# Performance work log

Measured on AMD Instinct MI355X. Metric: run time of the kernel, lower is better.

Reference implementation:

```python
import jax, jax.numpy as jnp
import numpy as np

B, C, H = 16, 512, 8
T_PI, T_P = 2048, 512  # mel frames, text tokens


def setup_inputs() -> dict:
    key = jax.random.key(0)
    ks = jax.random.split(key, 8)
    pi = jax.random.uniform(ks[0], (B, T_PI), dtype=jnp.float32) * T_P  # mel positions in text coords
    p = jax.random.uniform(ks[1], (B, T_P), dtype=jnp.float32) * T_P   # text positions
    x_h = jax.random.normal(ks[2], (B, C, T_P), dtype=jnp.float32)
    text_mask = jnp.ones((B, T_P), dtype=bool)
    sigma = jnp.ones((H,), dtype=jnp.float32) * 0.1
    w_hidden = jax.random.normal(ks[3], (2 * C, C), dtype=jnp.float32) / np.sqrt(C)
    b_hidden = jnp.zeros((2 * C,), dtype=jnp.float32)
    w_out = jax.random.normal(ks[4], (C, 2 * C), dtype=jnp.float32) / np.sqrt(2 * C)
    b_out = jnp.zeros((C,), dtype=jnp.float32)
    return {"pi": pi, "p": p, "x_h": x_h, "text_mask": text_mask,
            "sigma": sigma, "w_hidden": w_hidden, "b_hidden": b_hidden,
            "w_out": w_out, "b_out": b_out}


def reference(pi, p, x_h, text_mask, sigma, w_hidden, b_hidden, w_out, b_out):
    # Gaussian position-distance energies: (B, T_pi, T_p)
    energies = -(pi[:, :, None] - p[:, None, :]) ** 2
    real_sigma = jnp.clip(sigma, 1e-6, 3.0)  # (H,)
    # scale per head -> (B, H, T_pi, T_p)
    energies = energies[:, None, :, :] * real_sigma[None, :, None, None]
    energies = jnp.where(text_mask[:, None, None, :], energies, -jnp.inf)
    attns = jax.nn.softmax(energies, axis=-1)  # (B, H, T_pi, T_p)

    # 1x1 conv C -> 2C: h (B, 2C, T_p)
    h = jnp.einsum('oc,bct->bot', w_hidden, x_h) + b_hidden[None, :, None]
    Bh, twoC, Tp = h.shape
    nH = real_sigma.shape[0]
    d = twoC // nH
    h = h.reshape(Bh, nH, d, Tp).transpose(0, 1, 3, 2)  # (B, H, T_p, d)

    out = jnp.einsum('bhqt,bhtd->bhqd', attns, h)        # (B, H, T_pi, d)
    out = out.transpose(0, 1, 3, 2).reshape(Bh, twoC, -1)  # (B, 2C, T_pi)
    out = jnp.einsum('oc,bct->bot', w_out, out) + b_out[None, :, None]  # (B, C, T_pi)
    return (out, attns, real_sigma)
```

## Files before the change

kernel.cpp:

```cpp
#include <hip/hip_runtime.h>
#include <stdint.h>


typedef float  f32x4  __attribute__((ext_vector_type(4)));
typedef short  bf16x8 __attribute__((ext_vector_type(8)));

namespace {
constexpr int Bn = 16, Cc = 512, Hh = 8, TQ = 2048, TP = 512, Dd = 128, C2 = 1024;
constexpr size_t ATT_OFF = (size_t)Bn * Cc * TQ;
constexpr size_t SIG_OFF = ATT_OFF + (size_t)Bn * Hh * TQ * TP;
constexpr size_t XT_ELEMS  = (size_t)Bn * TP * Cc;
constexpr size_t WHB_ELEMS = (size_t)C2 * Cc;
constexpr size_t WOB_ELEMS = (size_t)Cc * C2;
constexpr size_t HWS_ELEMS = (size_t)Bn * Hh * Dd * TP;
constexpr size_t YWS_ELEMS = (size_t)Bn * TQ * C2;
}

__device__ inline ushort f2bf(float f) {
    uint32_t u = __float_as_uint(f);
    u += 0x7FFFu + ((u >> 16) & 1u);
    return (ushort)(u >> 16);
}

__device__ inline void gload16(const ushort* g, ushort* l) {
    __builtin_amdgcn_global_load_lds(
        (const __attribute__((address_space(1))) uint32_t*)g,
        (__attribute__((address_space(3))) uint32_t*)l, 16, 0, 0);
}

__global__ __launch_bounds__(256) void k_prep(
    const float* __restrict__ wh, const float* __restrict__ wo,
    const float* __restrict__ sg,
    ushort* __restrict__ whb, ushort* __restrict__ wob, float* __restrict__ sigo)
{
    int i = blockIdx.x * 256 + threadIdx.x;
    float4 a = *reinterpret_cast<const float4*>(&wh[(size_t)i * 4]);
    float4 b = *reinterpret_cast<const float4*>(&wo[(size_t)i * 4]);
    ushort4 ua, ub;
    ua.x = f2bf(a.x); ua.y = f2bf(a.y); ua.z = f2bf(a.z); ua.w = f2bf(a.w);
    ub.x = f2bf(b.x); ub.y = f2bf(b.y); ub.z = f2bf(b.z); ub.w = f2bf(b.w);
    *reinterpret_cast<ushort4*>(&whb[(size_t)i * 4]) = ua;
    *reinterpret_cast<ushort4*>(&wob[(size_t)i * 4]) = ub;
    if (i < Hh) sigo[i] = fminf(fmaxf(sg[i], 1e-6f), 3.0f);
}

__global__ __launch_bounds__(256) void k_xt(
    const float* __restrict__ x, ushort* __restrict__ xT)
{
    __shared__ float tile[64 * 67];
    int bid = blockIdx.x;
    int tt = bid & 7, cb = (bid >> 3) & 7, b = bid >> 6;
    int c0 = cb * 64, t0 = tt * 64;
    int tid = threadIdx.x;
    #pragma unroll
    for (int it = 0; it < 4; ++it) {
        int idx = it * 256 + tid;
        int rc = idx >> 4, tc = (idx & 15) * 4;
        float4 v = *reinterpret_cast<const float4*>(
            &x[((size_t)b * Cc + c0 + rc) * TP + t0 + tc]);
        tile[rc * 67 + tc + 0] = v.x; tile[rc * 67 + tc + 1] = v.y;
        tile[rc * 67 + tc + 2] = v.z; tile[rc * 67 + tc + 3] = v.w;
    }
    __syncthreads();
    #pragma unroll
    for (int it = 0; it < 4; ++it) {
        int idx = it * 256 + tid;
        int rt = idx >> 4, cc = (idx & 15) * 4;
        ushort4 o;
        o.x = f2bf(tile[(cc + 0) * 67 + rt]);
        o.y = f2bf(tile[(cc + 1) * 67 + rt]);
        o.z = f2bf(tile[(cc + 2) * 67 + rt]);
        o.w = f2bf(tile[(cc + 3) * 67 + rt]);
        *reinterpret_cast<ushort4*>(&xT[((size_t)b * TP + t0 + rt) * Cc + c0 + cc]) = o;
    }
}


__device__ __forceinline__ void hidden_role(
    int hid, ushort* pool, int tid,
    const ushort* xT, const ushort* whb, const float* bias, ushort* hws)
{
    int l = tid & 63, w = tid >> 6;
    int ot = hid & 15, tt = (hid >> 4) & 7, b = hid >> 7;
    int o0 = ot * 64, t0 = tt * 64;
    ushort* As = pool;
    ushort* Bs = pool + 4096;
    float* bias_s = reinterpret_cast<float*>(pool + 8192);
    if (tid < 64) bias_s[tid] = bias[o0 + tid];

    int wn = w * 16;
    int r = l & 15, g = l >> 4;
    f32x4 acc[4];
    #pragma unroll
    for (int m = 0; m < 4; ++m) acc[m] = (f32x4){0.f, 0.f, 0.f, 0.f};

    const ushort* ag = xT + ((size_t)b * TP + t0) * Cc;
    const ushort* bg = whb + (size_t)o0 * Cc;

    for (int k0 = 0; k0 < Cc; k0 += 64) {
        __syncthreads();
        #pragma unroll
        for (int it = 0; it < 2; ++it) {
            int idx = it * 256 + tid;
            int row = idx >> 3, ch = idx & 7;
            int dst = row * 64 + ((ch ^ (row & 7)) * 8);
            *reinterpret_cast<bf16x8*>(&As[dst]) =
                *reinterpret_cast<const bf16x8*>(&ag[(size_t)row * Cc + k0 + ch * 8]);
            *reinterpret_cast<bf16x8*>(&Bs[dst]) =
                *reinterpret_cast<const bf16x8*>(&bg[(size_t)row * Cc + k0 + ch * 8]);
        }
        __syncthreads();
        #pragma unroll
        for (int s = 0; s < 2; ++s) {
            int brow = wn + r;
            bf16x8 bv = *reinterpret_cast<const bf16x8*>(
                &Bs[brow * 64 + (((s * 4 + g) ^ (brow & 7)) * 8)]);
            #pragma unroll
            for (int m = 0; m < 4; ++m) {
                int row = m * 16 + r;
                bf16x8 av = *reinterpret_cast<const bf16x8*>(
                    &As[row * 64 + (((s * 4 + g) ^ (row & 7)) * 8)]);
                acc[m] = __builtin_amdgcn_mfma_f32_16x16x32_bf16(av, bv, acc[m], 0, 0, 0);
            }
        }
    }
    int og = o0 + wn + r;
    int hh = og >> 7, d = og & 127;
    float bi = bias_s[wn + r];
    #pragma unroll
    for (int m = 0; m < 4; ++m) {
        int t = t0 + m * 16 + g * 4;
        ushort4 v;
        v.x = f2bf(acc[m][0] + bi); v.y = f2bf(acc[m][1] + bi);
        v.z = f2bf(acc[m][2] + bi); v.w = f2bf(acc[m][3] + bi);
        *reinterpret_cast<ushort4*>(&hws[(((size_t)b * Hh + hh) * Dd + d) * TP + t]) = v;
    }
}

__device__ __forceinline__ void attw_role(
    int sub, int bbase, ushort* pool, int tid,
    const float* pi, const float* p, const float* sgm,
    float* attns, float2* nrm)
{
    float* p_s   = reinterpret_cast<float*>(pool);
    float* pim_s = reinterpret_cast<float*>(pool) + 512;
    int l = tid & 63, w = tid >> 6;
    int qt = sub & 31, hh = (sub >> 5) & 7, b = bbase + (sub >> 8);
    int q0 = qt * 64;
    float sig = fminf(fmaxf(sgm[hh], 1e-6f), 3.0f), nsig = -sig;

    for (int i = tid; i < TP; i += 256) p_s[i] = p[(size_t)b * TP + i];
    if (tid < 64) pim_s[tid] = pi[(size_t)b * TQ + q0 + tid];
    __syncthreads();

    float* abase = attns + (((size_t)b * Hh + hh) * TQ + q0) * TP;
    float2* nbase = nrm + ((size_t)b * Hh + hh) * TQ + q0;

    for (int rr = 0; rr < 16; ++rr) {
        int qloc = w * 16 + rr;
        float piq = pim_s[qloc];
        float d2[8];
        #pragma unroll
        for (int i = 0; i < 8; ++i) { float df = piq - p_s[l + 64 * i]; d2[i] = df * df; }
        float dmin = d2[0];
        #pragma unroll
        for (int i = 1; i < 8; ++i) dmin = fminf(dmin, d2[i]);
        #pragma unroll
        for (int off = 32; off; off >>= 1) dmin = fminf(dmin, __shfl_xor(dmin, off));
        float negm = sig * dmin;
        float vv[8], ssum = 0.f;
        #pragma unroll
        for (int i = 0; i < 8; ++i) { vv[i] = __expf(fmaf(d2[i], nsig, negm)); ssum += vv[i]; }
        #pragma unroll
        for (int off = 32; off; off >>= 1) ssum += __shfl_xor(ssum, off);
        float inv = 1.0f / ssum;
        if (l == 0) nbase[qloc] = make_float2(negm, inv);
        float* aptr = abase + (size_t)qloc * TP + l;
        #pragma unroll
        for (int i = 0; i < 8; ++i)
            __builtin_nontemporal_store(vv[i] * inv, &aptr[64 * i]);
    }
}

__device__ __forceinline__ void pv_role(
    int sub, int bbase, ushort* pool, int tid,
    const float* pi, const float* p, const float* sgm,
    const ushort* hws, const float2* nrm, ushort* y)
{
    float* p_s    = reinterpret_cast<float*>(pool);
    float* pim_s  = reinterpret_cast<float*>(pool + 1024);
    float* negm_s = reinterpret_cast<float*>(pool + 1152);
    float* inv_s  = reinterpret_cast<float*>(pool + 1280);
    ushort* Ht    = pool + 1408;
    ushort* yst_b = pool + 1408;

    int l = tid & 63, w = tid >> 6;
    int qt = sub & 31, hh = (sub >> 5) & 7, b = bbase + (sub >> 8);
    int q0 = qt * 64;
    float sig = fminf(fmaxf(sgm[hh], 1e-6f), 3.0f), nsig = -sig;

    const ushort* hb = hws + (size_t)(b * Hh + hh) * Dd * TP;
    int srow = l >> 3, sch = l & 7;

    for (int i = tid; i < TP; i += 256) p_s[i] = p[(size_t)b * TP + i];
    if (tid < 64) {
        pim_s[tid] = pi[(size_t)b * TQ + q0 + tid];
        float2 nv = nrm[((size_t)b * Hh + hh) * TQ + q0 + tid];
        negm_s[tid] = nv.x; inv_s[tid] = nv.y;
    }
    __syncthreads();

    int r = l & 15, g = l >> 4;
    int qloc = w * 16 + r;
    float piq = pim_s[qloc], negm = negm_s[qloc];
    f32x4 acc[8];
    #pragma unroll
    for (int n = 0; n < 8; ++n) acc[n] = (f32x4){0.f, 0.f, 0.f, 0.f};

    for (int tt = 0; tt < TP; tt += 64) {
        __syncthreads();
        #pragma unroll
        for (int it = 0; it < 4; ++it) {
            int c = w + it * 4;
            int row = c * 8 + srow;
            int chs = sch ^ (row & 7);
            gload16(&hb[(size_t)row * TP + tt + chs * 8], &Ht[c * 512]);
        }
        __syncthreads();
        #pragma unroll
        for (int s = 0; s < 2; ++s) {
            int tb = tt + s * 32 + g * 8;
            float4 pv0 = *reinterpret_cast<const float4*>(&p_s[tb]);
            float4 pv1 = *reinterpret_cast<const float4*>(&p_s[tb + 4]);
            float pvv[8] = {pv0.x, pv0.y, pv0.z, pv0.w, pv1.x, pv1.y, pv1.z, pv1.w};
            bf16x8 af;
            #pragma unroll
            for (int j = 0; j < 8; ++j) {
                float df = piq - pvv[j];
                af[j] = (short)f2bf(__expf(fmaf(df * df, nsig, negm)));
            }
            #pragma unroll
            for (int n = 0; n < 8; ++n) {
                int row = n * 16 + r;
                bf16x8 bv = *reinterpret_cast<const bf16x8*>(
                    &Ht[row * 64 + (((s * 4 + g) ^ (row & 7)) * 8)]);
                acc[n] = __builtin_amdgcn_mfma_f32_16x16x32_bf16(af, bv, acc[n], 0, 0, 0);
            }
        }
    }
    __syncthreads();

    float inv4[4];
    #pragma unroll
    for (int j = 0; j < 4; ++j) inv4[j] = inv_s[w * 16 + g * 4 + j];
    ushort* yst = yst_b + w * (16 * 132);
    #pragma unroll
    for (int n = 0; n < 8; ++n)
        #pragma unroll
        for (int j = 0; j < 4; ++j)
            yst[(g * 4 + j) * 132 + n * 16 + r] = f2bf(acc[n][j] * inv4[j]);
    __syncthreads();
    size_t ybase = (size_t)b * TQ + q0 + w * 16;
    #pragma unroll
    for (int it = 0; it < 4; ++it) {
        int idx = it * 64 + l;
        int qr = idx >> 4, c8 = (idx & 15) * 8;
        *reinterpret_cast<bf16x8*>(&y[(ybase + qr) * C2 + hh * Dd + c8]) =
            *reinterpret_cast<const bf16x8*>(&yst_b[w * (16 * 132) + qr * 132 + c8]);
    }
}

__device__ __forceinline__ void out_role(
    int oid, int bbase, ushort* pool, int tid,
    const ushort* y, const ushort* wob, const float* bout, float* outp)
{
    ushort* As = pool;
    ushort* Bs = pool + 8192;
    float* bo_s = reinterpret_cast<float*>(pool + 16384);

    int no = oid & 3, mq = (oid >> 2) & 15, b = bbase + (oid >> 6);
    int q0 = mq * 128, o0 = no * 128;
    int l = tid & 63, w = tid >> 6;
    int wm = (w >> 1) * 64, wn = (w & 1) * 64;
    int r = l & 15, g = l >> 4;
    if (tid < 128) bo_s[tid] = bout[o0 + tid];

    int srow = (l >> 3);
    int sch  = l & 7;

    f32x4 acc[4][4];
    #pragma unroll
    for (int m = 0; m < 4; ++m)
        #pragma unroll
        for (int n = 0; n < 4; ++n) acc[m][n] = (f32x4){0.f, 0.f, 0.f, 0.f};

    const ushort* agbase = y + ((size_t)b * TQ + q0) * C2;
    const ushort* bgbase = wob + (size_t)o0 * C2;

    for (int k0 = 0; k0 < C2; k0 += 64) {
        __syncthreads();
        #pragma unroll
        for (int it = 0; it < 4; ++it) {
            int c = w + it * 4;
            int row = c * 8 + srow;
            int chs = sch ^ (row & 7);
            gload16(&agbase[(size_t)row * C2 + k0 + chs * 8], &As[c * 512]);
            gload16(&bgbase[(size_t)row * C2 + k0 + chs * 8], &Bs[c * 512]);
        }
        __syncthreads();
        #pragma unroll
        for (int s = 0; s < 2; ++s) {
            bf16x8 av[4], bv[4];
            #pragma unroll
            for (int m = 0; m < 4; ++m) {
                int row = wm + m * 16 + r;
                av[m] = *reinterpret_cast<const bf16x8*>(
                    &As[row * 64 + (((s * 4 + g) ^ (row & 7)) * 8)]);
            }
            #pragma unroll
            for (int n = 0; n < 4; ++n) {
                int row = wn + n * 16 + r;
                bv[n] = *reinterpret_cast<const bf16x8*>(
                    &Bs[row * 64 + (((s * 4 + g) ^ (row & 7)) * 8)]);
            }
            #pragma unroll
            for (int m = 0; m < 4; ++m)
                #pragma unroll
                for (int n = 0; n < 4; ++n)
                    acc[m][n] = __builtin_amdgcn_mfma_f32_16x16x32_bf16(
                        av[m], bv[n], acc[m][n], 0, 0, 0);
        }
    }
    #pragma unroll
    for (int n = 0; n < 4; ++n) {
        int ol = wn + n * 16 + r;
        float bo = bo_s[ol];
        size_t obase = ((size_t)b * Cc + o0 + ol) * TQ + q0 + wm;
        #pragma unroll
        for (int m = 0; m < 4; ++m) {
            float4 v = make_float4(acc[m][n][0] + bo, acc[m][n][1] + bo,
                                   acc[m][n][2] + bo, acc[m][n][3] + bo);
            *reinterpret_cast<float4*>(&outp[obase + m * 16 + g * 4]) = v;
        }
    }
}

__global__ __launch_bounds__(256) void k_ha(
    const ushort* __restrict__ xT, const ushort* __restrict__ whb,
    const float* __restrict__ bias,
    const float* __restrict__ pi, const float* __restrict__ p,
    const float* __restrict__ sgm,
    ushort* __restrict__ hws, float* __restrict__ attns, float2* __restrict__ nrm)
{
    __shared__ __align__(16) ushort pool[8320];
    int bid = blockIdx.x, tid = threadIdx.x;
    int tri = bid >> 1;
    if ((bid & 1) == 0) hidden_role(tri, pool, tid, xT, whb, bias, hws);
    else                attw_role(tri, 0, pool, tid, pi, p, sgm, attns, nrm);
}

__global__ __launch_bounds__(256) void k_apv(
    const float* __restrict__ pi, const float* __restrict__ p,
    const float* __restrict__ sgm, const ushort* __restrict__ hws,
    float* __restrict__ attns, float2* __restrict__ nrm, ushort* __restrict__ y)
{
    __shared__ __align__(16) ushort pool[9856];
    int bid = blockIdx.x, tid = threadIdx.x;
    int tri = bid >> 1;
    if ((bid & 1) == 0) attw_role(tri, 8, pool, tid, pi, p, sgm, attns, nrm);
    else                pv_role(tri, 0, pool, tid, pi, p, sgm, hws, nrm, y);
}

__global__ __launch_bounds__(256) void k_pvout(
    const float* __restrict__ pi, const float* __restrict__ p,
    const float* __restrict__ sgm, const ushort* __restrict__ hws,
    const float2* __restrict__ nrm, ushort* __restrict__ y,
    const ushort* __restrict__ wob, const float* __restrict__ bout,
    float* __restrict__ outp)
{
    __shared__ __align__(16) ushort pool[16640];
    int bid = blockIdx.x, tid = threadIdx.x;
    int tri = bid / 5, rem = bid - tri * 5;
    if (rem == 0) out_role(tri, 0, pool, tid, y, wob, bout, outp);
    else          pv_role(tri * 4 + rem - 1, 8, pool, tid, pi, p, sgm, hws, nrm, y);
}

__global__ __launch_bounds__(256) void k_out2(
    const ushort* __restrict__ y, const ushort* __restrict__ wob,
    const float* __restrict__ bout, float* __restrict__ outp)
{
    __shared__ __align__(16) ushort pool[16640];
    out_role(blockIdx.x, 8, pool, threadIdx.x, y, wob, bout, outp);
}

extern "C" void kernel_launch(void* const* d_in, const int* in_sizes, int n_in,
                              void* d_out, int out_size, void* d_ws, size_t ws_size,
                              hipStream_t stream) {
    const float* pi    = (const float*)d_in[0];
    const float* p     = (const float*)d_in[1];
    const float* x_h   = (const float*)d_in[2];
    const float* sigma = (const float*)d_in[4];
    const float* w_h   = (const float*)d_in[5];
    const float* b_h   = (const float*)d_in[6];
    const float* w_o   = (const float*)d_in[7];
    const float* b_o   = (const float*)d_in[8];

    float* outp  = (float*)d_out;
    float* attns = outp + ATT_OFF;
    float* sigo  = outp + SIG_OFF;

    ushort* xT  = (ushort*)d_ws;
    ushort* whb = xT + XT_ELEMS;
    ushort* wob = whb + WHB_ELEMS;
    ushort* hws = wob + WOB_ELEMS;
    ushort* yws = hws + HWS_ELEMS;
    float2* nrm = (float2*)(yws + YWS_ELEMS);

    k_prep  <<<512,  256, 0, stream>>>(w_h, w_o, sigma, whb, wob, sigo);
    k_xt    <<<1024, 256, 0, stream>>>(x_h, xT);
    k_ha    <<<4096, 256, 0, stream>>>(xT, whb, b_h, pi, p, sigma, hws, attns, nrm);
    k_apv   <<<4096, 256, 0, stream>>>(pi, p, sigma, hws, attns, nrm, yws);
    k_pvout <<<2560, 256, 0, stream>>>(pi, p, sigma, hws, nrm, yws, wob, b_o, outp);
    k_out2  <<<512,  256, 0, stream>>>(yws, wob, b_o, outp);
}
```

Baseline: 232.8 us.

## Merge prep/transpose kernels and rebalance role ratios across fused stage kernels

Fuses the weight-conversion and x-transpose kernels into one launch with role dispatch by block index. It also changes how work is split between the fused stage kernels. More attention-weight tiles move into the first stage, and more PV and output tiles move into the middle stages, so the tail kernel shrinks. The aim is to cut launch overhead and keep each stage's mixed roles better balanced. The risk is that any wrong index arithmetic in the new role splits would leave tiles uncovered or computed twice.

```diff
diff --git a/kernel.cpp b/kernel.cpp
--- a/kernel.cpp
+++ b/kernel.cpp
@@ -28,12 +28,13 @@
         (__attribute__((address_space(3))) uint32_t*)l, 16, 0, 0);
 }
 
-__global__ __launch_bounds__(256) void k_prep(
-    const float* __restrict__ wh, const float* __restrict__ wo,
-    const float* __restrict__ sg,
-    ushort* __restrict__ whb, ushort* __restrict__ wob, float* __restrict__ sigo)
-{
-    int i = blockIdx.x * 256 + threadIdx.x;
+
+__device__ __forceinline__ void prep_role(
+    int pid, int tid,
+    const float* wh, const float* wo, const float* sg,
+    ushort* whb, ushort* wob, float* sigo)
+{
+    int i = pid * 256 + tid;
     float4 a = *reinterpret_cast<const float4*>(&wh[(size_t)i * 4]);
     float4 b = *reinterpret_cast<const float4*>(&wo[(size_t)i * 4]);
     ushort4 ua, ub;
@@ -44,14 +45,13 @@
     if (i < Hh) sigo[i] = fminf(fmaxf(sg[i], 1e-6f), 3.0f);
 }
 
-__global__ __launch_bounds__(256) void k_xt(
-    const float* __restrict__ x, ushort* __restrict__ xT)
-{
-    __shared__ float tile[64 * 67];
-    int bid = blockIdx.x;
-    int tt = bid & 7, cb = (bid >> 3) & 7, b = bid >> 6;
+__device__ __forceinline__ void xt_role(
+    int xid, ushort* poolu, int tid,
+    const float* x, ushort* xT)
+{
+    float* tile = reinterpret_cast<float*>(poolu);
+    int tt = xid & 7, cb = (xid >> 3) & 7, b = xid >> 6;
     int c0 = cb * 64, t0 = tt * 64;
-    int tid = threadIdx.x;
     #pragma unroll
     for (int it = 0; it < 4; ++it) {
         int idx = it * 256 + tid;
@@ -75,7 +75,6 @@
     }
 }
 
-
 __device__ __forceinline__ void hidden_role(
     int hid, ushort* pool, int tid,
     const ushort* xT, const ushort* whb, const float* bias, ushort* hws)
@@ -345,6 +344,18 @@
     }
 }
 
+__global__ __launch_bounds__(256) void k_px(
+    const float* __restrict__ wh, const float* __restrict__ wo,
+    const float* __restrict__ sg, const float* __restrict__ x,
+    ushort* __restrict__ whb, ushort* __restrict__ wob,
+    float* __restrict__ sigo, ushort* __restrict__ xT)
+{
+    __shared__ __align__(16) ushort pool[8576];
+    int bid = blockIdx.x, tid = threadIdx.x;
+    if (bid < 512) prep_role(bid, tid, wh, wo, sg, whb, wob, sigo);
+    else           xt_role(bid - 512, pool, tid, x, xT);
+}
+
 __global__ __launch_bounds__(256) void k_ha(
     const ushort* __restrict__ xT, const ushort* __restrict__ whb,
     const float* __restrict__ bias,
@@ -354,9 +365,9 @@
 {
     __shared__ __align__(16) ushort pool[8320];
     int bid = blockIdx.x, tid = threadIdx.x;
-    int tri = bid >> 1;
-    if ((bid & 1) == 0) hidden_role(tri, pool, tid, xT, whb, bias, hws);
-    else                attw_role(tri, 0, pool, tid, pi, p, sgm, attns, nrm);
+    int tri = bid / 9, rem = bid - tri * 9;
+    if (rem < 4) hidden_role(tri * 4 + rem, pool, tid, xT, whb, bias, hws);
+    else         attw_role(tri * 5 + rem - 4, 0, pool, tid, pi, p, sgm, attns, nrm);
 }
 
 __global__ __launch_bounds__(256) void k_apv(
@@ -366,9 +377,9 @@
 {
     __shared__ __align__(16) ushort pool[9856];
     int bid = blockIdx.x, tid = threadIdx.x;
-    int tri = bid >> 1;
-    if ((bid & 1) == 0) attw_role(tri, 8, pool, tid, pi, p, sgm, attns, nrm);
-    else                pv_role(tri, 0, pool, tid, pi, p, sgm, hws, nrm, y);
+    int tri = bid >> 3, rem = bid & 7;
+    if (rem < 3) attw_role(tri * 3 + rem, 10, pool, tid, pi, p, sgm, attns, nrm);
+    else         pv_role(tri * 5 + rem - 3, 0, pool, tid, pi, p, sgm, hws, nrm, y);
 }
 
 __global__ __launch_bounds__(256) void k_pvout(
@@ -380,9 +391,9 @@
 {
     __shared__ __align__(16) ushort pool[16640];
     int bid = blockIdx.x, tid = threadIdx.x;
-    int tri = bid / 5, rem = bid - tri * 5;
-    if (rem == 0) out_role(tri, 0, pool, tid, y, wob, bout, outp);
-    else          pv_role(tri * 4 + rem - 1, 8, pool, tid, pi, p, sgm, hws, nrm, y);
+    int tri = bid / 17, rem = bid - tri * 17;
+    if (rem < 5) out_role(tri * 5 + rem, 0, pool, tid, y, wob, bout, outp);
+    else         pv_role(tri * 12 + rem - 5, 10, pool, tid, pi, p, sgm, hws, nrm, y);
 }
 
 __global__ __launch_bounds__(256) void k_out2(
@@ -390,7 +401,7 @@
     const float* __restrict__ bout, float* __restrict__ outp)
 {
     __shared__ __align__(16) ushort pool[16640];
-    out_role(blockIdx.x, 8, pool, threadIdx.x, y, wob, bout, outp);
+    out_role(blockIdx.x, 10, pool, threadIdx.x, y, wob, bout, outp);
 }
 
 extern "C" void kernel_launch(void* const* d_in, const int* in_sizes, int n_in,
@@ -416,10 +427,9 @@
     ushort* yws = hws + HWS_ELEMS;
     float2* nrm = (float2*)(yws + YWS_ELEMS);
 
-    k_prep  <<<512,  256, 0, stream>>>(w_h, w_o, sigma, whb, wob, sigo);
-    k_xt    <<<1024, 256, 0, stream>>>(x_h, xT);
-    k_ha    <<<4096, 256, 0, stream>>>(xT, whb, b_h, pi, p, sigma, hws, attns, nrm);
+    k_px    <<<1536, 256, 0, stream>>>(w_h, w_o, sigma, x_h, whb, wob, sigo, xT);
+    k_ha    <<<4608, 256, 0, stream>>>(xT, whb, b_h, pi, p, sigma, hws, attns, nrm);
     k_apv   <<<4096, 256, 0, stream>>>(pi, p, sigma, hws, attns, nrm, yws);
-    k_pvout <<<2560, 256, 0, stream>>>(pi, p, sigma, hws, nrm, yws, wob, b_o, outp);
-    k_out2  <<<512,  256, 0, stream>>>(yws, wob, b_o, outp);
-}
+    k_pvout <<<2176, 256, 0, stream>>>(pi, p, sigma, hws, nrm, yws, wob, b_o, outp);
+    k_out2  <<<384,  256, 0, stream>>>(yws, wob, b_o, outp);
+}
```

New measurement: 250.7 us. +7.7%, slower.
